# Kernel optimization log

Measured on AMD Instinct MI355X. Metric: run time of the kernel, lower is better.

Reference implementation:

```python
import jax, jax.numpy as jnp
import numpy as np

D_MODEL = 1024
HIDDEN = 4096
NUM_EXPERTS = 8
TOP_K = 2
N_TOKENS = 4 * 2048  # batch * seq


def setup_inputs() -> dict:
    key = jax.random.key(0)
    k_x, k_w, k_i, k1, k2, k3 = jax.random.split(key, 6)
    x = jax.random.normal(k_x, (4, 2048, D_MODEL), dtype=jnp.float32)
    expert_weights = jax.random.uniform(k_w, (N_TOKENS, TOP_K), dtype=jnp.float32)
    expert_indices = jax.random.randint(k_i, (N_TOKENS, TOP_K), 0, NUM_EXPERTS)
    scale = 1.0 / np.sqrt(D_MODEL)
    w1 = jax.random.normal(k1, (NUM_EXPERTS, D_MODEL, HIDDEN), dtype=jnp.float32) * scale
    w3 = jax.random.normal(k3, (NUM_EXPERTS, D_MODEL, HIDDEN), dtype=jnp.float32) * scale
    w2 = jax.random.normal(k2, (NUM_EXPERTS, HIDDEN, D_MODEL), dtype=jnp.float32) * (1.0 / np.sqrt(HIDDEN))
    return {"x": x, "expert_weights": expert_weights, "expert_indices": expert_indices,
            "w1": w1, "w2": w2, "w3": w3}


def reference(x, expert_weights, expert_indices, w1, w2, w3):
    # forward_once of ParallelDroplessMLP (single-rank dropless MoE).
    in_shape = x.shape
    d_model = x.shape[-1]
    num_experts = w1.shape[0]
    xf = x.reshape(-1, d_model)                        # (N, d)
    top_k = expert_weights.shape[-1]
    ew = expert_weights.reshape(-1)                    # (N*top_k,)
    ei = expert_indices.reshape(-1).astype(jnp.int32)  # (N*top_k,)

    # indices_and_bins: stable sort by expert id + histogram
    order = jnp.argsort(ei)                            # (T,) permuted row -> flat (token, k) slot
    tokens_per_expert = jnp.bincount(ei, length=num_experts).astype(jnp.int32)

    # gather: replicate each token top_k times, grouped by expert
    token_of_row = order // top_k                      # (T,)
    xg = jnp.take(xf, token_of_row, axis=0)            # (T, d)

    # grouped GEMM (MegaBlocks-style) SwiGLU per expert via ragged_dot
    h = jax.nn.silu(jax.lax.ragged_dot(xg, w1, tokens_per_expert)) \
        * jax.lax.ragged_dot(xg, w3, tokens_per_expert)            # (T, hidden)
    y = jax.lax.ragged_dot(h, w2, tokens_per_expert)               # (T, d)

    # scatter: weighted un-permute back to token positions
    y = y * ew[order][:, None]
    out = jnp.zeros_like(xf).at[token_of_row].add(y)
    return out.reshape(in_shape), tokens_per_expert
```

## Files before the change

### kernel.cpp

```cpp
#include <hip/hip_runtime.h>

#define NTOK 8192
#define TROWS 16384
#define DM 1024
#define HID 4096
#define NEXP 8
#define MAXT256 72
#define MAXT128 136

typedef __bf16 bf16x8 __attribute__((ext_vector_type(8)));
typedef float  f32x4  __attribute__((ext_vector_type(4)));
typedef short  s16x4  __attribute__((ext_vector_type(4)));

#define BAR() do { asm volatile("" ::: "memory"); __builtin_amdgcn_s_barrier(); asm volatile("" ::: "memory"); } while(0)
#define VM6() asm volatile("s_waitcnt vmcnt(6)" ::: "memory")
#define VM0() asm volatile("s_waitcnt vmcnt(0)" ::: "memory")

__device__ __forceinline__ short f2bf(float f) {
  union { float f; unsigned u; } v; v.f = f;
  unsigned r = (v.u + 0x7fffu + ((v.u >> 16) & 1u)) >> 16;
  return (short)r;
}
__device__ __forceinline__ float bf2f(short s) {
  union { unsigned u; float f; } z; z.u = ((unsigned)(unsigned short)s) << 16; return z.f;
}

__device__ __forceinline__ void gload16(const short* g, short* l) {
  __builtin_amdgcn_global_load_lds(
      (const __attribute__((address_space(1))) void*)g,
      (__attribute__((address_space(3))) void*)l, 16, 0, 0);
}

__global__ void k_meta(const int* __restrict__ ei, int* __restrict__ meta,
                       float* __restrict__ outCounts) {
  __shared__ int c[NEXP];
  int tid = threadIdx.x;
  if (tid < NEXP) c[tid] = 0;
  __syncthreads();
  for (int i = tid; i < TROWS; i += 256) atomicAdd(&c[ei[i]], 1);
  __syncthreads();
  if (tid == 0) {
    int off = 0, s = 0, s2 = 0;
    for (int e = 0; e < NEXP; ++e) {
      int ce = c[e];
      meta[e] = ce;
      meta[8 + e] = off;
      meta[16 + e] = off;
      outCounts[e] = (float)ce;
      for (int r0 = 0; r0 < ce; r0 += 256) {
        meta[32 + 3*s] = e; meta[32 + 3*s + 1] = off + r0;
        meta[32 + 3*s + 2] = (ce - r0 < 256) ? (ce - r0) : 256; ++s;
      }
      for (int r0 = 0; r0 < ce; r0 += 128) {
        meta[256 + 3*s2] = e; meta[256 + 3*s2 + 1] = off + r0;
        meta[256 + 3*s2 + 2] = (ce - r0 < 128) ? (ce - r0) : 128; ++s2;
      }
      off += ce;
    }
    for (; s < MAXT256; ++s)  { meta[32 + 3*s] = 0;  meta[32 + 3*s + 1] = 0;  meta[32 + 3*s + 2] = 0; }
    for (; s2 < MAXT128; ++s2){ meta[256 + 3*s2] = 0; meta[256 + 3*s2 + 1] = 0; meta[256 + 3*s2 + 2] = 0; }
  }
}

__global__ void k_scatter(const int* __restrict__ ei, int* __restrict__ meta,
                          int* __restrict__ rowmap, int* __restrict__ inv) {
  int t = blockIdx.x * blockDim.x + threadIdx.x;
  if (t < TROWS) {
    int e = ei[t];
    int p = atomicAdd(&meta[16 + e], 1);
    rowmap[p] = t;
    inv[t] = p;
  }
}

__global__ void k_prep(const float* __restrict__ w1, const float* __restrict__ w3,
                       const float* __restrict__ w2, const float* __restrict__ x,
                       short* __restrict__ w1t, short* __restrict__ w3t,
                       short* __restrict__ w2t, short* __restrict__ xb) {
  int b = blockIdx.x;
  int which = b >> 13;
  if (which == 3) {
    int i = (b - 24576) * 256 + threadIdx.x;
    f32x4 v = ((const f32x4*)x)[i];
    s16x4 s = { f2bf(v.x), f2bf(v.y), f2bf(v.z), f2bf(v.w) };
    ((s16x4*)xb)[i] = s;
    return;
  }
  __shared__ float lt[64][65];
  int r = b & 8191;
  const float* in; short* out; int R, C;
  if (which == 0)      { in = w1; out = w1t; R = DM;  C = HID; }
  else if (which == 1) { in = w3; out = w3t; R = DM;  C = HID; }
  else                 { in = w2; out = w2t; R = HID; C = DM;  }
  int nx = C >> 6;
  int e = r >> 10;
  int rem = r & 1023;
  int c0 = (rem & (nx - 1)) * 64, r0 = (rem / nx) * 64;

  int t = threadIdx.x;
  int rr = t >> 4, cc = (t & 15) * 4;
  const float* src = in + ((size_t)e * R + r0 + rr) * C + c0 + cc;
#pragma unroll
  for (int i = 0; i < 4; ++i)
    *(f32x4*)&lt[rr + i*16][cc] = *(const f32x4*)(src + (size_t)i * 16 * C);
  __syncthreads();
  int cN = t >> 4, r4 = (t & 15) * 4;
  short* dst = out + ((size_t)e * C + c0 + cN) * R + r0 + r4;
#pragma unroll
  for (int i = 0; i < 4; ++i) {
    s16x4 o;
#pragma unroll
    for (int j = 0; j < 4; ++j) o[j] = f2bf(lt[r4 + j][cN + i*16]);
    *(s16x4*)(dst + (size_t)i * 16 * R) = o;
  }
}

__global__ __launch_bounds__(512, 2) void k_gemm1(
    const short* __restrict__ xb, const short* __restrict__ w1t, const short* __restrict__ w3t,
    const int* __restrict__ rowmap, const int* __restrict__ meta, short* __restrict__ hbuf) {
  int bid = blockIdx.x;
  int xcd = bid & 7, rk = bid >> 3;
  int slot = xcd * 9 + (rk >> 5);
  int bn   = rk & 31;
  int rows = meta[32 + 3*slot + 2];
  if (rows <= 0) return;
  int e    = meta[32 + 3*slot];
  int row0 = meta[32 + 3*slot + 1];

  __shared__ short lA [2][256 * 64];
  __shared__ short lB1[2][128 * 64];
  __shared__ short lB3[2][128 * 64];

  int tid = threadIdx.x, l = tid & 63, w = tid >> 6;
  int wr = (w >> 2) * 128, wc = (w & 3) * 32;
  int lr = l & 15, cb = (l >> 4) * 16, axor = (lr & 7) << 4;
  int srow = l >> 3;
  int scol = ((l & 7) ^ srow) * 8;

  const short* aG[2][2];
#pragma unroll
  for (int h = 0; h < 2; ++h)
#pragma unroll
    for (int i = 0; i < 2; ++i) {
      int r = h*128 + w*16 + i*8 + srow;
      int rc = r < rows ? r : rows - 1;
      int tok = rowmap[row0 + rc] >> 1;
      aG[h][i] = xb + (size_t)tok * DM + scol;
    }
  const short *b1G[2], *b3G[2];
#pragma unroll
  for (int i = 0; i < 2; ++i) {
    size_t grow = (size_t)e * HID + (size_t)bn * 128 + w*16 + i*8 + srow;
    b1G[i] = w1t + grow * DM + scol;
    b3G[i] = w3t + grow * DM + scol;
  }

  f32x4 acc1[2][4][2], acc3[2][4][2];
#pragma unroll
  for (int h = 0; h < 2; ++h)
#pragma unroll
    for (int i = 0; i < 4; ++i)
#pragma unroll
      for (int j = 0; j < 2; ++j) {
        acc1[h][i][j] = (f32x4){0.f,0.f,0.f,0.f};
        acc3[h][i][j] = (f32x4){0.f,0.f,0.f,0.f};
      }

  auto stgA = [&](int buf, int h, int kt) {
    gload16(aG[h][0] + kt, &lA[buf][(h*128 + w*16    ) * 64]);
    gload16(aG[h][1] + kt, &lA[buf][(h*128 + w*16 + 8) * 64]);
  };
  auto stgB1 = [&](int buf, int kt) {
    gload16(b1G[0] + kt, &lB1[buf][(w*16    ) * 64]);
    gload16(b1G[1] + kt, &lB1[buf][(w*16 + 8) * 64]);
  };
  auto stgB3 = [&](int buf, int kt) {
    gload16(b3G[0] + kt, &lB3[buf][(w*16    ) * 64]);
    gload16(b3G[1] + kt, &lB3[buf][(w*16 + 8) * 64]);
  };

  stgA(0, 0, 0); stgA(0, 1, 0); stgB1(0, 0); stgB3(0, 0);
  stgB1(1, 64); stgB3(1, 64); stgA(1, 0, 64);
  VM6();
  BAR();

  const int NT = DM / 64;
  int c = 0;
  for (int t = 0; t < NT; ++t, c ^= 1) {
    int kn  = t*64 + 64;
    int kn2 = t*64 + 128;
    const char* cA  = (const char*)&lA [c][0];
    const char* cB1 = (const char*)&lB1[c][0];
    const char* cB3 = (const char*)&lB3[c][0];

    bf16x8 alo[4][2], b1w[2][2];
#pragma unroll
    for (int i = 0; i < 4; ++i)
#pragma unroll
      for (int kk = 0; kk < 2; ++kk)
        alo[i][kk] = *(const bf16x8*)(cA + (wr + i*16 + lr)*128 + ((kk*64 + cb) ^ axor));
#pragma unroll
    for (int j = 0; j < 2; ++j)
#pragma unroll
      for (int kk = 0; kk < 2; ++kk)
        b1w[j][kk] = *(const bf16x8*)(cB1 + (wc + j*16 + lr)*128 + ((kk*64 + cb) ^ axor));
    if (t + 1 < NT) stgA(c ^ 1, 1, kn);
    BAR();
    __builtin_amdgcn_s_setprio(1);
#pragma unroll
    for (int i = 0; i < 4; ++i)
#pragma unroll
      for (int j = 0; j < 2; ++j)
#pragma unroll
        for (int kk = 0; kk < 2; ++kk)
          acc1[0][i][j] = __builtin_amdgcn_mfma_f32_16x16x32_bf16(alo[i][kk], b1w[j][kk], acc1[0][i][j], 0, 0, 0);
    __builtin_amdgcn_s_setprio(0);
    BAR();

    bf16x8 b3w[2][2];
#pragma unroll
    for (int j = 0; j < 2; ++j)
#pragma unroll
      for (int kk = 0; kk < 2; ++kk)
        b3w[j][kk] = *(const bf16x8*)(cB3 + (wc + j*16 + lr)*128 + ((kk*64 + cb) ^ axor));
    if (t + 2 < NT) stgB1(c, kn2);
    BAR();
    __builtin_amdgcn_s_setprio(1);
#pragma unroll
    for (int i = 0; i < 4; ++i)
#pragma unroll
      for (int j = 0; j < 2; ++j)
#pragma unroll
        for (int kk = 0; kk < 2; ++kk)
          acc3[0][i][j] = __builtin_amdgcn_mfma_f32_16x16x32_bf16(alo[i][kk], b3w[j][kk], acc3[0][i][j], 0, 0, 0);
    __builtin_amdgcn_s_setprio(0);
    BAR();

    bf16x8 ahi[4][2];
#pragma unroll
    for (int i = 0; i < 4; ++i)
#pragma unroll
      for (int kk = 0; kk < 2; ++kk)
        ahi[i][kk] = *(const bf16x8*)(cA + (wr + 64 + i*16 + lr)*128 + ((kk*64 + cb) ^ axor));
    if (t + 2 < NT) stgB3(c, kn2);
    BAR();
    __builtin_amdgcn_s_setprio(1);
#pragma unroll
    for (int i = 0; i < 4; ++i)
#pragma unroll
      for (int j = 0; j < 2; ++j)
#pragma unroll
        for (int kk = 0; kk < 2; ++kk)
          acc1[1][i][j] = __builtin_amdgcn_mfma_f32_16x16x32_bf16(ahi[i][kk], b1w[j][kk], acc1[1][i][j], 0, 0, 0);
    __builtin_amdgcn_s_setprio(0);
    BAR();

    if (t + 2 < NT) stgA(c, 0, kn2);
    __builtin_amdgcn_s_setprio(1);
#pragma unroll
    for (int i = 0; i < 4; ++i)
#pragma unroll
      for (int j = 0; j < 2; ++j)
#pragma unroll
        for (int kk = 0; kk < 2; ++kk)
          acc3[1][i][j] = __builtin_amdgcn_mfma_f32_16x16x32_bf16(ahi[i][kk], b3w[j][kk], acc3[1][i][j], 0, 0, 0);
    __builtin_amdgcn_s_setprio(0);
    if (t < NT - 2) { VM6(); } else { VM0(); }
    BAR();
  }

#pragma unroll
  for (int h = 0; h < 2; ++h)
#pragma unroll
    for (int i = 0; i < 4; ++i)
#pragma unroll
      for (int q = 0; q < 4; ++q) {
        int r = wr + h*64 + i*16 + (l >> 4)*4 + q;
        if (r < rows) {
          size_t base = (size_t)(row0 + r) * HID + (size_t)bn * 128 + wc;
#pragma unroll
          for (int j = 0; j < 2; ++j) {
            float g = acc1[h][i][j][q], u3 = acc3[h][i][j][q];
            float sv = g / (1.f + __expf(-g));
            hbuf[base + j*16 + lr] = f2bf(sv * u3);
          }
        }
      }
}

__global__ __launch_bounds__(256) void k_gemm2(
    const short* __restrict__ hbuf, const short* __restrict__ w2t,
    const int* __restrict__ meta, short* __restrict__ y) {
  int bid = blockIdx.x;
  int xcd = bid & 7, rk = bid >> 3;
  int slot = xcd * 17 + (rk >> 3);
  int bn   = rk & 7;
  int rows = meta[256 + 3*slot + 2];
  if (rows <= 0) return;
  int e    = meta[256 + 3*slot];
  int row0 = meta[256 + 3*slot + 1];

  __shared__ short lA[128 * 64];
  __shared__ short lB[128 * 64];

  int tid = threadIdx.x;
  int l = tid & 63, w = tid >> 6;

  int srow = w*8 + (l >> 3);
  int scol = ((l & 7) ^ (l >> 3)) * 8;

  const short* aG[4];
  for (int p = 0; p < 4; ++p) {
    int r = p*32 + srow;
    int rc = r < rows ? r : rows - 1;
    aG[p] = hbuf + (size_t)(row0 + rc) * HID + scol;
  }
  const short* bG[4];
  for (int p = 0; p < 4; ++p) {
    size_t grow = (size_t)e * DM + (size_t)bn * 128 + p*32 + srow;
    bG[p] = w2t + grow * HID + scol;
  }

  f32x4 acc[4][4];
  for (int i = 0; i < 4; ++i)
    for (int j = 0; j < 4; ++j) acc[i][j] = (f32x4){0.f, 0.f, 0.f, 0.f};

  int wr = (w >> 1) * 64, wc = (w & 1) * 64;
  int lr = l & 15;
  int cb = (l >> 4) * 16;
  int axor = (lr & 7) << 4;

  for (int kt = 0; kt < HID; kt += 64) {
#pragma unroll
    for (int p = 0; p < 4; ++p) {
      gload16(aG[p] + kt, &lA[(p*32 + w*8) * 64]);
      gload16(bG[p] + kt, &lB[(p*32 + w*8) * 64]);
    }
    __syncthreads();
#pragma unroll
    for (int kk2 = 0; kk2 < 2; ++kk2) {
      int co = (kk2*64 + cb) ^ axor;
      bf16x8 a[4], b[4];
#pragma unroll
      for (int i = 0; i < 4; ++i) a[i] = *(const bf16x8*)((const char*)lA + (wr + i*16 + lr)*128 + co);
#pragma unroll
      for (int j = 0; j < 4; ++j) b[j] = *(const bf16x8*)((const char*)lB + (wc + j*16 + lr)*128 + co);
#pragma unroll
      for (int i = 0; i < 4; ++i)
#pragma unroll
        for (int j = 0; j < 4; ++j)
          acc[i][j] = __builtin_amdgcn_mfma_f32_16x16x32_bf16(a[i], b[j], acc[i][j], 0, 0, 0);
    }
    __syncthreads();
  }

  for (int i = 0; i < 4; ++i)
    for (int q = 0; q < 4; ++q) {
      int r = wr + i*16 + (l >> 4)*4 + q;
      if (r < rows) {
        size_t obase = (size_t)(row0 + r) * DM + (size_t)bn * 128 + wc;
        for (int j = 0; j < 4; ++j)
          y[obase + j*16 + lr] = f2bf(acc[i][j][q]);
      }
    }
}

__global__ void k_unperm(const short* __restrict__ y, const int* __restrict__ inv,
                         const float* __restrict__ ew, float* __restrict__ out) {
  int i = blockIdx.x * 256 + threadIdx.x;
  int tok = i >> 8, c = i & 255;
  int p0 = inv[2*tok], p1 = inv[2*tok + 1];
  float w0 = ew[2*tok], w1v = ew[2*tok + 1];
  s16x4 a = ((const s16x4*)y)[(size_t)p0 * 256 + c];
  s16x4 b = ((const s16x4*)y)[(size_t)p1 * 256 + c];
  f32x4 r;
#pragma unroll
  for (int j = 0; j < 4; ++j) r[j] = w0 * bf2f(a[j]) + w1v * bf2f(b[j]);
  ((f32x4*)out)[i] = r;
}

extern "C" void kernel_launch(void* const* d_in, const int* in_sizes, int n_in,
                              void* d_out, int out_size, void* d_ws, size_t ws_size,
                              hipStream_t stream) {
  const float* x  = (const float*)d_in[0];
  const float* ew = (const float*)d_in[1];
  const int*   ei = (const int*)d_in[2];
  const float* w1 = (const float*)d_in[3];
  const float* w2 = (const float*)d_in[4];
  const float* w3 = (const float*)d_in[5];
  float* out = (float*)d_out;
  char*  ws  = (char*)d_ws;

  short* w1t = (short*)(ws + 0);
  short* w3t = (short*)(ws + 67108864);
  short* w2t = (short*)(ws + 134217728);
  short* xb  = (short*)(ws + 201326592);
  short* hb  = (short*)(ws + 218103808);
  int*   meta   = (int*)(ws + 352321536);
  int*   rowmap = (int*)(ws + 352321536 + 8192);
  int*   inv    = (int*)(ws + 352321536 + 73728);
  short* y      = (short*)(ws + 0);

  k_meta<<<1, 256, 0, stream>>>(ei, meta, out + (size_t)NTOK * DM);
  k_scatter<<<TROWS / 256, 256, 0, stream>>>(ei, meta, rowmap, inv);
  k_prep<<<32768, 256, 0, stream>>>(w1, w3, w2, x, w1t, w3t, w2t, xb);
  k_gemm1<<<MAXT256 * (HID/128), 512, 0, stream>>>(xb, w1t, w3t, rowmap, meta, hb);
  k_gemm2<<<MAXT128 * (DM/128), 256, 0, stream>>>(hb, w2t, meta, y);
  k_unperm<<<NTOK * DM / 4 / 256, 256, 0, stream>>>(y, inv, ew, out);
}
```

Before: 743.8 us.

## Parallelize expert histogram, remap gemm1 tile swizzle, widen unpermute loads

```diff
diff --git a/kernel.cpp b/kernel.cpp
--- a/kernel.cpp
+++ b/kernel.cpp
@@ -11,6 +11,7 @@
 typedef __bf16 bf16x8 __attribute__((ext_vector_type(8)));
 typedef float  f32x4  __attribute__((ext_vector_type(4)));
 typedef short  s16x4  __attribute__((ext_vector_type(4)));
+typedef short  s16x8  __attribute__((ext_vector_type(8)));
 
 #define BAR() do { asm volatile("" ::: "memory"); __builtin_amdgcn_s_barrier(); asm volatile("" ::: "memory"); } while(0)
 #define VM6() asm volatile("s_waitcnt vmcnt(6)" ::: "memory")
@@ -31,35 +32,37 @@
       (__attribute__((address_space(3))) void*)l, 16, 0, 0);
 }
 
-__global__ void k_meta(const int* __restrict__ ei, int* __restrict__ meta,
-                       float* __restrict__ outCounts) {
+
+__global__ void k_histo(const int* __restrict__ ei, int* __restrict__ meta) {
+  int t = blockIdx.x * 256 + threadIdx.x;
   __shared__ int c[NEXP];
-  int tid = threadIdx.x;
-  if (tid < NEXP) c[tid] = 0;
+  if (threadIdx.x < NEXP) c[threadIdx.x] = 0;
   __syncthreads();
-  for (int i = tid; i < TROWS; i += 256) atomicAdd(&c[ei[i]], 1);
+  atomicAdd(&c[ei[t]], 1);
   __syncthreads();
-  if (tid == 0) {
-    int off = 0, s = 0, s2 = 0;
-    for (int e = 0; e < NEXP; ++e) {
-      int ce = c[e];
-      meta[e] = ce;
-      meta[8 + e] = off;
-      meta[16 + e] = off;
-      outCounts[e] = (float)ce;
-      for (int r0 = 0; r0 < ce; r0 += 256) {
-        meta[32 + 3*s] = e; meta[32 + 3*s + 1] = off + r0;
-        meta[32 + 3*s + 2] = (ce - r0 < 256) ? (ce - r0) : 256; ++s;
-      }
-      for (int r0 = 0; r0 < ce; r0 += 128) {
-        meta[256 + 3*s2] = e; meta[256 + 3*s2 + 1] = off + r0;
-        meta[256 + 3*s2 + 2] = (ce - r0 < 128) ? (ce - r0) : 128; ++s2;
-      }
-      off += ce;
-    }
-    for (; s < MAXT256; ++s)  { meta[32 + 3*s] = 0;  meta[32 + 3*s + 1] = 0;  meta[32 + 3*s + 2] = 0; }
-    for (; s2 < MAXT128; ++s2){ meta[256 + 3*s2] = 0; meta[256 + 3*s2 + 1] = 0; meta[256 + 3*s2 + 2] = 0; }
-  }
+  if (threadIdx.x < NEXP) atomicAdd(&meta[threadIdx.x], c[threadIdx.x]);
+}
+
+__global__ void k_plan(int* __restrict__ meta, float* __restrict__ outCounts) {
+  if (threadIdx.x != 0 || blockIdx.x != 0) return;
+  int off = 0, s = 0, s2 = 0;
+  for (int e = 0; e < NEXP; ++e) {
+    int ce = meta[e];
+    meta[8 + e] = off;
+    meta[16 + e] = off;
+    outCounts[e] = (float)ce;
+    for (int r0 = 0; r0 < ce; r0 += 256) {
+      meta[32 + 3*s] = e; meta[32 + 3*s + 1] = off + r0;
+      meta[32 + 3*s + 2] = (ce - r0 < 256) ? (ce - r0) : 256; ++s;
+    }
+    for (int r0 = 0; r0 < ce; r0 += 128) {
+      meta[256 + 3*s2] = e; meta[256 + 3*s2 + 1] = off + r0;
+      meta[256 + 3*s2 + 2] = (ce - r0 < 128) ? (ce - r0) : 128; ++s2;
+    }
+    off += ce;
+  }
+  for (; s < MAXT256; ++s)  { meta[32 + 3*s] = 0;  meta[32 + 3*s + 1] = 0;  meta[32 + 3*s + 2] = 0; }
+  for (; s2 < MAXT128; ++s2){ meta[256 + 3*s2] = 0; meta[256 + 3*s2 + 1] = 0; meta[256 + 3*s2 + 2] = 0; }
 }
 
 __global__ void k_scatter(const int* __restrict__ ei, int* __restrict__ meta,
@@ -119,9 +122,9 @@
     const short* __restrict__ xb, const short* __restrict__ w1t, const short* __restrict__ w3t,
     const int* __restrict__ rowmap, const int* __restrict__ meta, short* __restrict__ hbuf) {
   int bid = blockIdx.x;
-  int xcd = bid & 7, rk = bid >> 3;
-  int slot = xcd * 9 + (rk >> 5);
-  int bn   = rk & 31;
+  int swz = (bid & 7) * 288 + (bid >> 3);
+  int slot = swz % MAXT256;
+  int bn   = swz / MAXT256;
   int rows = meta[32 + 3*slot + 2];
   if (rows <= 0) return;
   int e    = meta[32 + 3*slot];
@@ -368,15 +371,18 @@
 __global__ void k_unperm(const short* __restrict__ y, const int* __restrict__ inv,
                          const float* __restrict__ ew, float* __restrict__ out) {
   int i = blockIdx.x * 256 + threadIdx.x;
-  int tok = i >> 8, c = i & 255;
+  int tok = i >> 7, c = i & 127;
   int p0 = inv[2*tok], p1 = inv[2*tok + 1];
   float w0 = ew[2*tok], w1v = ew[2*tok + 1];
-  s16x4 a = ((const s16x4*)y)[(size_t)p0 * 256 + c];
-  s16x4 b = ((const s16x4*)y)[(size_t)p1 * 256 + c];
-  f32x4 r;
-#pragma unroll
-  for (int j = 0; j < 4; ++j) r[j] = w0 * bf2f(a[j]) + w1v * bf2f(b[j]);
-  ((f32x4*)out)[i] = r;
+  s16x8 a = ((const s16x8*)y)[(size_t)p0 * 128 + c];
+  s16x8 b = ((const s16x8*)y)[(size_t)p1 * 128 + c];
+  f32x4 r0, r1;
+#pragma unroll
+  for (int j = 0; j < 4; ++j) r0[j] = w0 * bf2f(a[j])     + w1v * bf2f(b[j]);
+#pragma unroll
+  for (int j = 0; j < 4; ++j) r1[j] = w0 * bf2f(a[j + 4]) + w1v * bf2f(b[j + 4]);
+  ((f32x4*)out)[2*i]     = r0;
+  ((f32x4*)out)[2*i + 1] = r1;
 }
 
 extern "C" void kernel_launch(void* const* d_in, const int* in_sizes, int n_in,
@@ -401,10 +407,12 @@
   int*   inv    = (int*)(ws + 352321536 + 73728);
   short* y      = (short*)(ws + 0);
 
-  k_meta<<<1, 256, 0, stream>>>(ei, meta, out + (size_t)NTOK * DM);
+  hipMemsetAsync(meta, 0, NEXP * sizeof(int), stream);
+  k_histo<<<TROWS / 256, 256, 0, stream>>>(ei, meta);
+  k_plan<<<1, 64, 0, stream>>>(meta, out + (size_t)NTOK * DM);
   k_scatter<<<TROWS / 256, 256, 0, stream>>>(ei, meta, rowmap, inv);
   k_prep<<<32768, 256, 0, stream>>>(w1, w3, w2, x, w1t, w3t, w2t, xb);
   k_gemm1<<<MAXT256 * (HID/128), 512, 0, stream>>>(xb, w1t, w3t, rowmap, meta, hb);
   k_gemm2<<<MAXT128 * (DM/128), 256, 0, stream>>>(hb, w2t, meta, y);
-  k_unperm<<<NTOK * DM / 4 / 256, 256, 0, stream>>>(y, inv, ew, out);
-}
+  k_unperm<<<NTOK * DM / 8 / 256, 256, 0, stream>>>(y, inv, ew, out);
+}
```

New measurement: 712.0 us. 4.3% less time.
